# Optimization experiments

Measured on AMD Instinct MI355X. Metric: run time of the kernel, lower is better.

The kernel has to match this reference:

```python
import jax, jax.numpy as jnp
import numpy as np

BATCH, SEQ, EMBED = 4, 4096, 512
NUM_HEADS = 8
D_K = EMBED // NUM_HEADS  # = n_wires of the quantum layer


def setup_inputs() -> dict:
    key = jax.random.key(0)
    k1, k2, k3, k4 = jax.random.split(key, 4)
    x = jax.random.normal(k1, (BATCH, SEQ, EMBED), dtype=jnp.float32)
    theta = jax.random.normal(k2, (D_K,), dtype=jnp.float32)          # trainable RX angles (shared across heads)
    W_out = jax.random.normal(k3, (EMBED, EMBED), dtype=jnp.float32) * (1.0 / np.sqrt(EMBED))
    b_out = jax.random.normal(k4, (EMBED,), dtype=jnp.float32) * 0.01
    return {"x": x, "theta": theta, "W_out": W_out, "b_out": b_out}


def reference(x, theta, W_out, b_out):
    b, s, e = x.shape
    d_k = theta.shape[0]
    h = e // d_k
    # Quantum stage: per wire, RX(x_i) then RX(theta_i) on |0>, measure PauliZ.
    # RX gates on the same wire compose, and <Z| RX(phi)|0> state> = cos(phi),
    # so the whole per-head circuit is elementwise cos(x + theta).
    xh = x.reshape(b, s, h, d_k)                 # split heads
    q_concat = jnp.cos(xh + theta).reshape(b, s, e)
    # q = k = v = out_proj(q_concat)  (same Linear applied three times)
    q = q_concat @ W_out.T + b_out               # [b, s, e]
    scale = 1.0 / jnp.sqrt(jnp.asarray(d_k, dtype=q.dtype))
    scores = jax.nn.softmax(jnp.einsum('bie,bje->bij', q, q) * scale, axis=-1)  # [b, s, s]
    out = jnp.einsum('bij,bje->bie', scores, q)  # dropout = identity (inference)
    return out
```

## Files before the change

kernel.cpp:

```cpp
#include <hip/hip_runtime.h>

typedef __bf16 bf16_t;
typedef bf16_t bf16x8 __attribute__((ext_vector_type(8)));
typedef bf16_t bf16x4 __attribute__((ext_vector_type(4)));
typedef float f32x4 __attribute__((ext_vector_type(4)));

#define BATCH 4
#define SEQ 4096
#define EMBED 512
#define MTOT (BATCH * SEQ)
#define NSPLIT 2
#define KT (SEQ / NSPLIT)
#define BC 32
#define FITERS (KT / BC)

__device__ float  Lacc_g[MTOT];
__device__ bf16_t Wbf_g[EMBED * EMBED];

__device__ __forceinline__ void async_copy16(const bf16_t* g, bf16_t* l) {
    __builtin_amdgcn_global_load_lds(
        (const __attribute__((address_space(1))) unsigned int*)g,
        (__attribute__((address_space(3))) unsigned int*)l, 16, 0, 0);
}

__global__ __launch_bounds__(256) void cvt_w_kernel(const float* __restrict__ W) {
    const int i = (blockIdx.x * 256 + threadIdx.x) * 4;
    float4 v = *(const float4*)&W[i];
    bf16x4 o;
    o[0] = (bf16_t)v.x; o[1] = (bf16_t)v.y; o[2] = (bf16_t)v.z; o[3] = (bf16_t)v.w;
    *(bf16x4*)&Wbf_g[i] = o;
    if (blockIdx.x < 16)
        ((float4*)Lacc_g)[blockIdx.x * 256 + threadIdx.x] = make_float4(0.f, 0.f, 0.f, 0.f);
}

__global__ __launch_bounds__(256) void cvt_a_kernel(
    const float* __restrict__ x, const float* __restrict__ theta,
    bf16_t* __restrict__ abuf)
{
    const int i = (blockIdx.x * 256 + threadIdx.x) * 8;
    float4 a = *(const float4*)&x[i];
    float4 b = *(const float4*)&x[i + 4];
    const int e0 = i & 63;
    bf16x8 o;
    o[0] = (bf16_t)__cosf(a.x + theta[e0 + 0]);
    o[1] = (bf16_t)__cosf(a.y + theta[e0 + 1]);
    o[2] = (bf16_t)__cosf(a.z + theta[e0 + 2]);
    o[3] = (bf16_t)__cosf(a.w + theta[e0 + 3]);
    o[4] = (bf16_t)__cosf(b.x + theta[e0 + 4]);
    o[5] = (bf16_t)__cosf(b.y + theta[e0 + 5]);
    o[6] = (bf16_t)__cosf(b.z + theta[e0 + 6]);
    o[7] = (bf16_t)__cosf(b.w + theta[e0 + 7]);
    *(bf16x8*)&abuf[i] = o;
}

__global__ __launch_bounds__(256, 2) void gemm_q_kernel(
    const bf16_t* __restrict__ abuf, const float* __restrict__ bias,
    bf16_t* __restrict__ kperm, bf16_t* __restrict__ qt)
{
    __shared__ alignas(16) bf16_t As[128 * 64];
    __shared__ alignas(16) bf16_t Bs[128 * 64];
    __shared__ alignas(16) bf16_t Es[128 * 136];

    const int t    = threadIdx.x;
    const int lane = t & 63;
    const int wave = t >> 6;
    const int l15  = lane & 15;
    const int quad = lane >> 4;
    const int m0   = (blockIdx.x >> 2) * 128;
    const int n0   = (blockIdx.x & 3) * 128;
    const int wm   = wave >> 1;
    const int wn   = wave & 1;

    const int drow = lane >> 3;
    const int dseg = lane & 7;
    const int sseg = dseg ^ drow;

    f32x4 acc[4][4];
#pragma unroll
    for (int mt = 0; mt < 4; ++mt)
#pragma unroll
        for (int nt = 0; nt < 4; ++nt) acc[mt][nt] = (f32x4){0.f, 0.f, 0.f, 0.f};

    for (int kk = 0; kk < 8; ++kk) {
        const int k0 = kk * 64;
        __syncthreads();
#pragma unroll
        for (int j = 0; j < 4; ++j) {
            const int c   = wave * 4 + j;
            const int row = c * 8 + drow;
            async_copy16(&abuf[(size_t)(m0 + row) * 512 + k0 + sseg * 8], &As[c * 512]);
            async_copy16(&Wbf_g[(size_t)(n0 + row) * 512 + k0 + sseg * 8], &Bs[c * 512]);
        }
        __syncthreads();
#pragma unroll
        for (int kh = 0; kh < 2; ++kh) {
            bf16x8 af[4], bfr[4];
#pragma unroll
            for (int i = 0; i < 4; ++i) {
                const int rA = wm * 64 + i * 16 + l15;
                const int rB = wn * 64 + i * 16 + l15;
                const int sg = kh * 4 + quad;
                af[i]  = *(const bf16x8*)&As[rA * 64 + (sg ^ (rA & 7)) * 8];
                bfr[i] = *(const bf16x8*)&Bs[rB * 64 + (sg ^ (rB & 7)) * 8];
            }
#pragma unroll
            for (int mt = 0; mt < 4; ++mt)
#pragma unroll
                for (int nt = 0; nt < 4; ++nt)
                    acc[mt][nt] = __builtin_amdgcn_mfma_f32_16x16x32_bf16(af[mt], bfr[nt], acc[mt][nt], 0, 0, 0);
        }
    }

    const int b     = m0 >> 12;
    const int mloc  = m0 & 4095;

#pragma unroll
    for (int nt = 0; nt < 4; ++nt) {
        const int colL = wn * 64 + nt * 16 + l15;
        const float bv = bias[n0 + colL];
        const int kfL = colL >> 5;
        const int inc = ((colL >> 3) & 3) * 128 + (colL & 7);
#pragma unroll
        for (int mt = 0; mt < 4; ++mt) {
            const int rowL0 = wm * 64 + mt * 16 + quad * 4;
            const int c     = (rowL0 >> 5) * 8 + ((rowL0 >> 4) & 1) * 4 + kfL;
            const int base  = c * 512 + inc + (rowL0 & 15) * 8;
#pragma unroll
            for (int r = 0; r < 4; ++r)
                Es[base + r * 8] = (bf16_t)(acc[mt][nt][r] + bv);
        }
    }
    __syncthreads();
    {
        const int tileB = mloc >> 5;
        const int kfB   = n0 >> 5;
#pragma unroll
        for (int p = 0; p < 8; ++p) {
            const int flat = p * 256 + t;
            const int c2   = flat >> 6;
            const int off  = (flat & 63) * 8;
            const int tile = c2 >> 3;
            const int mh   = (c2 >> 2) & 1;
            const int kfL2 = c2 & 3;
            const size_t dst = (size_t)b * (SEQ * EMBED)
                             + (size_t)(tileB + tile) * 16384
                             + (size_t)(mh * 16 + kfB + kfL2) * 512 + off;
            *(bf16x8*)&kperm[dst] = *(const bf16x8*)&Es[c2 * 512 + off];
        }
    }
    __syncthreads();
#pragma unroll
    for (int nt = 0; nt < 4; ++nt) {
        const int colL = wn * 64 + nt * 16 + l15;
        const float bv = bias[n0 + colL];
#pragma unroll
        for (int mt = 0; mt < 4; ++mt) {
            const int rowL0 = wm * 64 + mt * 16 + quad * 4;
#pragma unroll
            for (int r = 0; r < 4; ++r)
                Es[colL * 136 + rowL0 + r] = (bf16_t)(acc[mt][nt][r] + bv);
        }
    }
    __syncthreads();
    {
#pragma unroll
        for (int p = 0; p < 8; ++p) {
            const int flat = p * 256 + t;
            const int col  = flat >> 4;
            const int sub  = flat & 15;
            *(bf16x8*)&qt[((size_t)(b * 512 + n0 + col) << 12) + mloc + sub * 8]
                = *(const bf16x8*)&Es[col * 136 + sub * 8];
        }
    }
}

__global__ __launch_bounds__(256, 2) void flash_kernel(
    const bf16_t* __restrict__ kp, const bf16_t* __restrict__ qt,
    float* __restrict__ out)
{
    __shared__ alignas(16) bf16_t Ks[2][32 * 512];
    __shared__ alignas(16) bf16_t Ps[2][4 * 512];

    const int t    = threadIdx.x;
    const int lane = t & 63;
    const int wave = t >> 6;
    const int l15  = lane & 15;
    const int quad = lane >> 4;

    const int L      = blockIdx.x;
    const int g      = L & 7;
    const int qtile  = L >> 3;
    const int batch  = g >> 1;
    const int ksplit = g & 1;

    const int q0     = qtile * 64;
    const int kbase  = ksplit * KT;
    const int ktile0 = kbase >> 5;
    const bf16_t* kpb = kp + (size_t)batch * SEQ * EMBED;
    const bf16_t* qtb = qt + (size_t)batch * EMBED * SEQ;

#pragma unroll
    for (int cc = 0; cc < 8; ++cc) {
        const int f = cc * 4 + wave;
        async_copy16(&kpb[(size_t)ktile0 * 16384 + f * 512 + lane * 8],
                     &Ks[0][f * 512]);
    }

    bf16x8 bQ[16];
    {
        const size_t qb = (size_t)(qtile * 2 + (wave >> 1)) * 16384
                        + (size_t)(wave & 1) * 16 * 512;
#pragma unroll
        for (int kf = 0; kf < 16; ++kf)
            bQ[kf] = *(const bf16x8*)&kpb[qb + kf * 512 + quad * 128 + l15 * 8];
    }

    f32x4 O[4][8];
#pragma unroll
    for (int m = 0; m < 4; ++m)
#pragma unroll
        for (int n = 0; n < 8; ++n) O[m][n] = (f32x4){0.f, 0.f, 0.f, 0.f};
    float lpart = 0.f;

    for (int it = 0; it < FITERS; ++it) {
        const int cbuf = it & 1;
        const int pbuf = cbuf ^ 1;
        __syncthreads();
        bf16x8 bv[8];
        if (it) {
            const int kv = kbase + (it - 1) * BC;
#pragma unroll
            for (int n = 0; n < 8; ++n)
                bv[n] = *(const bf16x8*)&qtb[(size_t)(wave * 128 + n * 16 + l15) * 4096
                                             + kv + quad * 8];
        }
        if (it + 1 < FITERS) {
#pragma unroll
            for (int cc = 0; cc < 8; ++cc) {
                const int f = cc * 4 + wave;
                async_copy16(&kpb[(size_t)(ktile0 + it + 1) * 16384 + f * 512 + lane * 8],
                             &Ks[pbuf][f * 512]);
            }
        }
        f32x4 s[2];
#pragma unroll
        for (int kt = 0; kt < 2; ++kt) {
            f32x4 a = (f32x4){0.f, 0.f, 0.f, 0.f};
#pragma unroll
            for (int kf = 0; kf < 16; ++kf) {
                bf16x8 ak = *(const bf16x8*)&Ks[cbuf][(kt * 16 + kf) * 512 + lane * 8];
                a = __builtin_amdgcn_mfma_f32_16x16x32_bf16(ak, bQ[kf], a, 0, 0, 0);
            }
            s[kt] = a;
        }
#pragma unroll
        for (int kt = 0; kt < 2; ++kt) {
            bf16x4 pk;
#pragma unroll
            for (int r = 0; r < 4; ++r) {
                bf16_t pb = (bf16_t)__expf(s[kt][r] * 0.125f);
                lpart += (float)pb;
                pk[r] = pb;
            }
            *(bf16x4*)&Ps[cbuf][wave * 512 + (kt * 2 + (quad >> 1)) * 128
                                + l15 * 8 + (quad & 1) * 4] = pk;
        }
        if (it) {
            bf16x8 pa[4];
#pragma unroll
            for (int mt = 0; mt < 4; ++mt)
                pa[mt] = *(const bf16x8*)&Ps[pbuf][mt * 512 + lane * 8];
            __builtin_amdgcn_s_setprio(1);
#pragma unroll
            for (int n = 0; n < 8; ++n)
#pragma unroll
                for (int mt = 0; mt < 4; ++mt)
                    O[mt][n] = __builtin_amdgcn_mfma_f32_16x16x32_bf16(pa[mt], bv[n], O[mt][n], 0, 0, 0);
            __builtin_amdgcn_s_setprio(0);
        }
    }
    __syncthreads();
    {
        const int pbuf = (FITERS - 1) & 1;
        const int kv = kbase + (FITERS - 1) * BC;
        bf16x8 bv[8];
#pragma unroll
        for (int n = 0; n < 8; ++n)
            bv[n] = *(const bf16x8*)&qtb[(size_t)(wave * 128 + n * 16 + l15) * 4096
                                         + kv + quad * 8];
        bf16x8 pa[4];
#pragma unroll
        for (int mt = 0; mt < 4; ++mt)
            pa[mt] = *(const bf16x8*)&Ps[pbuf][mt * 512 + lane * 8];
        __builtin_amdgcn_s_setprio(1);
#pragma unroll
        for (int n = 0; n < 8; ++n)
#pragma unroll
            for (int mt = 0; mt < 4; ++mt)
                O[mt][n] = __builtin_amdgcn_mfma_f32_16x16x32_bf16(pa[mt], bv[n], O[mt][n], 0, 0, 0);
        __builtin_amdgcn_s_setprio(0);
    }

    {
        float ls = lpart;
        ls += __shfl_xor(ls, 16);
        ls += __shfl_xor(ls, 32);
        if (quad == 0)
            atomicAdd(&Lacc_g[batch * SEQ + q0 + wave * 16 + l15], ls);
    }
#pragma unroll
    for (int mt = 0; mt < 4; ++mt)
#pragma unroll
        for (int r = 0; r < 4; ++r) {
            const size_t row = (size_t)batch * SEQ + q0 + mt * 16 + quad * 4 + r;
#pragma unroll
            for (int n = 0; n < 8; ++n)
                atomicAdd(&out[row * 512 + wave * 128 + n * 16 + l15], O[mt][n][r]);
        }
}

__global__ __launch_bounds__(256) void norm_kernel(float* __restrict__ out)
{
    const int idx = blockIdx.x * 256 + threadIdx.x;
    float4 v = ((float4*)out)[idx];
    const float inv = 1.0f / Lacc_g[idx >> 7];
    v.x *= inv; v.y *= inv; v.z *= inv; v.w *= inv;
    ((float4*)out)[idx] = v;
}

extern "C" void kernel_launch(void* const* d_in, const int* in_sizes, int n_in,
                              void* d_out, int out_size, void* d_ws, size_t ws_size,
                              hipStream_t stream) {
    const float* x     = (const float*)d_in[0];
    const float* theta = (const float*)d_in[1];
    const float* W     = (const float*)d_in[2];
    const float* bias  = (const float*)d_in[3];
    float* out    = (float*)d_out;
    bf16_t* kperm = (bf16_t*)d_ws;
    bf16_t* qt    = kperm + (size_t)MTOT * EMBED;
    bf16_t* abuf  = qt + (size_t)MTOT * EMBED;

    hipMemsetAsync(out, 0, (size_t)MTOT * EMBED * sizeof(float), stream);

    cvt_w_kernel<<<dim3(EMBED * EMBED / 4 / 256), dim3(256), 0, stream>>>(W);

    cvt_a_kernel<<<dim3(MTOT * EMBED / 8 / 256), dim3(256), 0, stream>>>(x, theta, abuf);

    gemm_q_kernel<<<dim3((MTOT / 128) * 4), dim3(256), 0, stream>>>(abuf, bias, kperm, qt);

    flash_kernel<<<dim3(64 * BATCH * NSPLIT), dim3(256), 0, stream>>>(kperm, qt, out);

    norm_kernel<<<dim3(MTOT * EMBED / 4 / 256), dim3(256), 0, stream>>>(out);
}
```

Measured before the change: 366.1 us.

## Drop key split, use 8-wave flash blocks with in-kernel normalization, double-buffer GEMM

The flash kernel no longer splits keys across two blocks. Each block now runs 8 waves over all 4096 keys: wave pairs share a query group, split the key tile for the scores, and split the output columns. Row sums are reduced in shared memory so outputs are normalized and written directly with nontemporal stores. This removes the output memset, the float atomics and the separate norm kernel. The Q-projection GEMM also double-buffers its async LDS loads to overlap loading with MFMA work, at the cost of more shared memory and half as many flash blocks (256 instead of 512).

```diff
diff --git a/kernel.cpp b/kernel.cpp
--- a/kernel.cpp
+++ b/kernel.cpp
@@ -9,12 +9,9 @@
 #define SEQ 4096
 #define EMBED 512
 #define MTOT (BATCH * SEQ)
-#define NSPLIT 2
-#define KT (SEQ / NSPLIT)
 #define BC 32
-#define FITERS (KT / BC)
-
-__device__ float  Lacc_g[MTOT];
+#define FITERS (SEQ / BC)
+
 __device__ bf16_t Wbf_g[EMBED * EMBED];
 
 __device__ __forceinline__ void async_copy16(const bf16_t* g, bf16_t* l) {
@@ -29,8 +26,6 @@
     bf16x4 o;
     o[0] = (bf16_t)v.x; o[1] = (bf16_t)v.y; o[2] = (bf16_t)v.z; o[3] = (bf16_t)v.w;
     *(bf16x4*)&Wbf_g[i] = o;
-    if (blockIdx.x < 16)
-        ((float4*)Lacc_g)[blockIdx.x * 256 + threadIdx.x] = make_float4(0.f, 0.f, 0.f, 0.f);
 }
 
 __global__ __launch_bounds__(256) void cvt_a_kernel(
@@ -57,9 +52,7 @@
     const bf16_t* __restrict__ abuf, const float* __restrict__ bias,
     bf16_t* __restrict__ kperm, bf16_t* __restrict__ qt)
 {
-    __shared__ alignas(16) bf16_t As[128 * 64];
-    __shared__ alignas(16) bf16_t Bs[128 * 64];
-    __shared__ alignas(16) bf16_t Es[128 * 136];
+    __shared__ alignas(16) bf16_t smem[4 * 8192];
 
     const int t    = threadIdx.x;
     const int lane = t & 63;
@@ -81,9 +74,9 @@
 #pragma unroll
         for (int nt = 0; nt < 4; ++nt) acc[mt][nt] = (f32x4){0.f, 0.f, 0.f, 0.f};
 
-    for (int kk = 0; kk < 8; ++kk) {
-        const int k0 = kk * 64;
-        __syncthreads();
+    auto stage = [&](int buf, int k0) {
+        bf16_t* As = smem + buf * 16384;
+        bf16_t* Bs = As + 8192;
 #pragma unroll
         for (int j = 0; j < 4; ++j) {
             const int c   = wave * 4 + j;
@@ -91,7 +84,15 @@
             async_copy16(&abuf[(size_t)(m0 + row) * 512 + k0 + sseg * 8], &As[c * 512]);
             async_copy16(&Wbf_g[(size_t)(n0 + row) * 512 + k0 + sseg * 8], &Bs[c * 512]);
         }
-        __syncthreads();
+    };
+
+    stage(0, 0);
+    __syncthreads();
+    int cur = 0;
+    for (int kk = 0; kk < 8; ++kk) {
+        if (kk + 1 < 8) stage(cur ^ 1, (kk + 1) * 64);
+        const bf16_t* As = smem + cur * 16384;
+        const bf16_t* Bs = As + 8192;
 #pragma unroll
         for (int kh = 0; kh < 2; ++kh) {
             bf16x8 af[4], bfr[4];
@@ -109,10 +110,13 @@
                 for (int nt = 0; nt < 4; ++nt)
                     acc[mt][nt] = __builtin_amdgcn_mfma_f32_16x16x32_bf16(af[mt], bfr[nt], acc[mt][nt], 0, 0, 0);
         }
+        __syncthreads();
+        cur ^= 1;
     }
 
     const int b     = m0 >> 12;
     const int mloc  = m0 & 4095;
+    bf16_t* Es = smem;
 
 #pragma unroll
     for (int nt = 0; nt < 4; ++nt) {
@@ -174,95 +178,97 @@
     }
 }
 
-__global__ __launch_bounds__(256, 2) void flash_kernel(
+__global__ __launch_bounds__(512, 2) void flash_kernel(
     const bf16_t* __restrict__ kp, const bf16_t* __restrict__ qt,
     float* __restrict__ out)
 {
     __shared__ alignas(16) bf16_t Ks[2][32 * 512];
     __shared__ alignas(16) bf16_t Ps[2][4 * 512];
+    __shared__ float Ls[8][16];
+    __shared__ float Lf[64];
 
     const int t    = threadIdx.x;
     const int lane = t & 63;
-    const int wave = t >> 6;
+    const int w    = t >> 6;
     const int l15  = lane & 15;
     const int quad = lane >> 4;
+    const int qg   = w >> 1;
+    const int ktw  = w & 1;
 
     const int L      = blockIdx.x;
-    const int g      = L & 7;
-    const int qtile  = L >> 3;
-    const int batch  = g >> 1;
-    const int ksplit = g & 1;
-
-    const int q0     = qtile * 64;
-    const int kbase  = ksplit * KT;
-    const int ktile0 = kbase >> 5;
+    const int xcd    = L & 7;
+    const int slot   = L >> 3;
+    const int batch  = xcd >> 1;
+    const int qtile  = (xcd & 1) * 32 + slot;
+
+    const int q0 = qtile * 64;
     const bf16_t* kpb = kp + (size_t)batch * SEQ * EMBED;
     const bf16_t* qtb = qt + (size_t)batch * EMBED * SEQ;
 
 #pragma unroll
-    for (int cc = 0; cc < 8; ++cc) {
-        const int f = cc * 4 + wave;
-        async_copy16(&kpb[(size_t)ktile0 * 16384 + f * 512 + lane * 8],
-                     &Ks[0][f * 512]);
+    for (int cc = 0; cc < 4; ++cc) {
+        const int f = cc * 8 + w;
+        async_copy16(&kpb[(size_t)f * 512 + lane * 8], &Ks[0][f * 512]);
     }
 
     bf16x8 bQ[16];
     {
-        const size_t qb = (size_t)(qtile * 2 + (wave >> 1)) * 16384
-                        + (size_t)(wave & 1) * 16 * 512;
+        const size_t qb = (size_t)(qtile * 2 + (qg >> 1)) * 16384
+                        + (size_t)(qg & 1) * 16 * 512;
 #pragma unroll
         for (int kf = 0; kf < 16; ++kf)
-            bQ[kf] = *(const bf16x8*)&kpb[qb + kf * 512 + quad * 128 + l15 * 8];
-    }
-
-    f32x4 O[4][8];
+            bQ[kf] = *(const bf16x8*)&kpb[qb + kf * 512 + lane * 8];
+    }
+
+    f32x4 O[4][4];
 #pragma unroll
     for (int m = 0; m < 4; ++m)
 #pragma unroll
-        for (int n = 0; n < 8; ++n) O[m][n] = (f32x4){0.f, 0.f, 0.f, 0.f};
+        for (int n = 0; n < 4; ++n) O[m][n] = (f32x4){0.f, 0.f, 0.f, 0.f};
     float lpart = 0.f;
 
     for (int it = 0; it < FITERS; ++it) {
         const int cbuf = it & 1;
         const int pbuf = cbuf ^ 1;
         __syncthreads();
-        bf16x8 bv[8];
+        bf16x8 bv[4];
         if (it) {
-            const int kv = kbase + (it - 1) * BC;
-#pragma unroll
-            for (int n = 0; n < 8; ++n)
-                bv[n] = *(const bf16x8*)&qtb[(size_t)(wave * 128 + n * 16 + l15) * 4096
+            const int kv = (it - 1) * BC;
+#pragma unroll
+            for (int n = 0; n < 4; ++n)
+                bv[n] = *(const bf16x8*)&qtb[(size_t)(w * 64 + n * 16 + l15) * 4096
                                              + kv + quad * 8];
         }
         if (it + 1 < FITERS) {
 #pragma unroll
-            for (int cc = 0; cc < 8; ++cc) {
-                const int f = cc * 4 + wave;
-                async_copy16(&kpb[(size_t)(ktile0 + it + 1) * 16384 + f * 512 + lane * 8],
+            for (int cc = 0; cc < 4; ++cc) {
+                const int f = cc * 8 + w;
+                async_copy16(&kpb[(size_t)(it + 1) * 16384 + f * 512 + lane * 8],
                              &Ks[pbuf][f * 512]);
             }
         }
-        f32x4 s[2];
-#pragma unroll
-        for (int kt = 0; kt < 2; ++kt) {
-            f32x4 a = (f32x4){0.f, 0.f, 0.f, 0.f};
-#pragma unroll
-            for (int kf = 0; kf < 16; ++kf) {
-                bf16x8 ak = *(const bf16x8*)&Ks[cbuf][(kt * 16 + kf) * 512 + lane * 8];
-                a = __builtin_amdgcn_mfma_f32_16x16x32_bf16(ak, bQ[kf], a, 0, 0, 0);
+        f32x4 s;
+        {
+            f32x4 a0 = (f32x4){0.f, 0.f, 0.f, 0.f};
+            f32x4 a1 = (f32x4){0.f, 0.f, 0.f, 0.f};
+#pragma unroll
+            for (int kf = 0; kf < 8; ++kf) {
+                bf16x8 ak0 = *(const bf16x8*)&Ks[cbuf][(ktw * 16 + kf) * 512 + lane * 8];
+                bf16x8 ak1 = *(const bf16x8*)&Ks[cbuf][(ktw * 16 + 8 + kf) * 512 + lane * 8];
+                a0 = __builtin_amdgcn_mfma_f32_16x16x32_bf16(ak0, bQ[kf],     a0, 0, 0, 0);
+                a1 = __builtin_amdgcn_mfma_f32_16x16x32_bf16(ak1, bQ[8 + kf], a1, 0, 0, 0);
             }
-            s[kt] = a;
-        }
-#pragma unroll
-        for (int kt = 0; kt < 2; ++kt) {
+            s = a0 + a1;
+        }
+        {
             bf16x4 pk;
 #pragma unroll
             for (int r = 0; r < 4; ++r) {
-                bf16_t pb = (bf16_t)__expf(s[kt][r] * 0.125f);
+                bf16_t pb = (bf16_t)__expf(s[r] * 0.125f);
                 lpart += (float)pb;
                 pk[r] = pb;
             }
-            *(bf16x4*)&Ps[cbuf][wave * 512 + (kt * 2 + (quad >> 1)) * 128
+            *(bf16x4*)&Ps[cbuf][qg * 512 + (ktw * 2 + (quad >> 1)) * 128
                                 + l15 * 8 + (quad & 1) * 4] = pk;
         }
         if (it) {
@@ -272,7 +278,7 @@
                 pa[mt] = *(const bf16x8*)&Ps[pbuf][mt * 512 + lane * 8];
             __builtin_amdgcn_s_setprio(1);
 #pragma unroll
-            for (int n = 0; n < 8; ++n)
+            for (int n = 0; n < 4; ++n)
 #pragma unroll
                 for (int mt = 0; mt < 4; ++mt)
                     O[mt][n] = __builtin_amdgcn_mfma_f32_16x16x32_bf16(pa[mt], bv[n], O[mt][n], 0, 0, 0);
@@ -282,11 +288,11 @@
     __syncthreads();
     {
         const int pbuf = (FITERS - 1) & 1;
-        const int kv = kbase + (FITERS - 1) * BC;
-        bf16x8 bv[8];
-#pragma unroll
-        for (int n = 0; n < 8; ++n)
-            bv[n] = *(const bf16x8*)&qtb[(size_t)(wave * 128 + n * 16 + l15) * 4096
+        const int kv = (FITERS - 1) * BC;
+        bf16x8 bv[4];
+#pragma unroll
+        for (int n = 0; n < 4; ++n)
+            bv[n] = *(const bf16x8*)&qtb[(size_t)(w * 64 + n * 16 + l15) * 4096
                                          + kv + quad * 8];
         bf16x8 pa[4];
 #pragma unroll
@@ -294,7 +300,7 @@
             pa[mt] = *(const bf16x8*)&Ps[pbuf][mt * 512 + lane * 8];
         __builtin_amdgcn_s_setprio(1);
 #pragma unroll
-        for (int n = 0; n < 8; ++n)
+        for (int n = 0; n < 4; ++n)
 #pragma unroll
             for (int mt = 0; mt < 4; ++mt)
                 O[mt][n] = __builtin_amdgcn_mfma_f32_16x16x32_bf16(pa[mt], bv[n], O[mt][n], 0, 0, 0);
@@ -305,27 +311,25 @@
         float ls = lpart;
         ls += __shfl_xor(ls, 16);
         ls += __shfl_xor(ls, 32);
-        if (quad == 0)
-            atomicAdd(&Lacc_g[batch * SEQ + q0 + wave * 16 + l15], ls);
-    }
+        if (lane < 16) Ls[w][lane] = ls;
+    }
+    __syncthreads();
+    if (t < 64)
+        Lf[t] = 1.0f / (Ls[(t >> 4) * 2][t & 15] + Ls[(t >> 4) * 2 + 1][t & 15]);
+    __syncthreads();
+
 #pragma unroll
     for (int mt = 0; mt < 4; ++mt)
 #pragma unroll
         for (int r = 0; r < 4; ++r) {
-            const size_t row = (size_t)batch * SEQ + q0 + mt * 16 + quad * 4 + r;
-#pragma unroll
-            for (int n = 0; n < 8; ++n)
-                atomicAdd(&out[row * 512 + wave * 128 + n * 16 + l15], O[mt][n][r]);
-        }
-}
-
-__global__ __launch_bounds__(256) void norm_kernel(float* __restrict__ out)
-{
-    const int idx = blockIdx.x * 256 + threadIdx.x;
-    float4 v = ((float4*)out)[idx];
-    const float inv = 1.0f / Lacc_g[idx >> 7];
-    v.x *= inv; v.y *= inv; v.z *= inv; v.w *= inv;
-    ((float4*)out)[idx] = v;
+            const int qloc = mt * 16 + quad * 4 + r;
+            const float inv = Lf[qloc];
+            const size_t row = (size_t)batch * SEQ + q0 + qloc;
+#pragma unroll
+            for (int n = 0; n < 4; ++n)
+                __builtin_nontemporal_store(O[mt][n][r] * inv,
+                    &out[row * 512 + w * 64 + n * 16 + l15]);
+        }
 }
 
 extern "C" void kernel_launch(void* const* d_in, const int* in_sizes, int n_in,
@@ -340,15 +344,11 @@
     bf16_t* qt    = kperm + (size_t)MTOT * EMBED;
     bf16_t* abuf  = qt + (size_t)MTOT * EMBED;
 
-    hipMemsetAsync(out, 0, (size_t)MTOT * EMBED * sizeof(float), stream);
-
     cvt_w_kernel<<<dim3(EMBED * EMBED / 4 / 256), dim3(256), 0, stream>>>(W);
 
     cvt_a_kernel<<<dim3(MTOT * EMBED / 8 / 256), dim3(256), 0, stream>>>(x, theta, abuf);
 
     gemm_q_kernel<<<dim3((MTOT / 128) * 4), dim3(256), 0, stream>>>(abuf, bias, kperm, qt);
 
-    flash_kernel<<<dim3(64 * BATCH * NSPLIT), dim3(256), 0, stream>>>(kperm, qt, out);
-
-    norm_kernel<<<dim3(MTOT * EMBED / 4 / 256), dim3(256), 0, stream>>>(out);
-}
+    flash_kernel<<<dim3(SEQ / 64 * BATCH), dim3(512), 0, stream>>>(kperm, qt, out);
+}
```

After: 339.0 us. -7.4%, faster.
